# Performance work log

Hardware: AMD Instinct MI355X
Metric: run time of the kernel (lower is better)

The kernel has to match this reference:

```python
import jax, jax.numpy as jnp
import numpy as np

N_USERS = 200000
N_ITEMS = 200000
HOPS = 4      # n_hops + 1
DIM = 64
BATCH = 2048
N_NEGS = 64
K = 2
DECAY = 1e-4


def setup_inputs() -> dict:
    key = jax.random.key(0)
    k1, k2, k3, k4, k5, k6 = jax.random.split(key, 6)
    return {
        "user_gcn_emb": jax.random.normal(k1, (N_USERS, HOPS, DIM), dtype=jnp.float32),
        "item_gcn_emb": jax.random.normal(k2, (N_ITEMS, HOPS, DIM), dtype=jnp.float32),
        "seed_embed": jax.random.normal(k3, (BATCH, 1), dtype=jnp.float32),
        "user": jax.random.randint(k4, (BATCH,), 0, N_USERS, dtype=jnp.int64 if jax.config.jax_enable_x64 else jnp.int32),
        "pos_item": jax.random.randint(k5, (BATCH,), 0, N_ITEMS, dtype=jnp.int64 if jax.config.jax_enable_x64 else jnp.int32),
        "neg_item": jax.random.randint(k6, (BATCH, K * N_NEGS), 0, N_ITEMS, dtype=jnp.int64 if jax.config.jax_enable_x64 else jnp.int32),
    }


def _negative_sampling(user_gcn_emb, item_gcn_emb, user, neg_candidates, pos_item, seed_embed):
    # s_e, p_e: [B, H, C]; n_e: [B, N, H, C]
    s_e = user_gcn_emb[user]
    p_e = item_gcn_emb[pos_item]
    n_e = item_gcn_emb[neg_candidates]
    seed = seed_embed[:, :, None, None]                      # [B,1,1,1]
    # positive mixing
    n_e_ = seed * p_e[:, None, :, :] + (1.0 - seed) * n_e    # [B,N,H,C]
    # hop mixing: per-hop inner product scores
    scores = jnp.einsum("bhc,bnhc->bnh", s_e, n_e_)          # [B,N,H]
    idx = jnp.argmax(scores, axis=1)                         # [B,H] (detached/int)
    # select per-hop hardest mixed negative
    sel = jnp.take_along_axis(n_e_, idx[:, None, :, None], axis=1)  # [B,1,H,C]
    return sel[:, 0]                                         # [B,H,C]


def _bpr_loss(user_e, pos_e_hops, neg_e_hops):
    # user_e/pos_e_hops: [B,H,C]; neg_e_hops: [B,K,H,C]
    B = user_e.shape[0]
    u_e = jnp.mean(user_e, axis=1)          # [B,C]  (pool='mean')
    pos_e = jnp.mean(pos_e_hops, axis=1)    # [B,C]
    neg_e = jnp.mean(neg_e_hops, axis=2)    # [B,K,C]
    pos_scores = jnp.sum(u_e * pos_e, axis=-1)              # [B]
    neg_scores = jnp.einsum("bc,bkc->bk", u_e, neg_e)       # [B,K]
    mf_loss = jnp.mean(jnp.log1p(jnp.sum(jnp.exp(neg_scores - pos_scores[:, None]), axis=1)))
    regularize = (jnp.sum(u_e ** 2) + jnp.sum(pos_e ** 2) + jnp.sum(neg_e ** 2)) / 2.0
    emb_loss = DECAY * regularize / B
    return mf_loss + emb_loss, mf_loss, emb_loss


def reference(user_gcn_emb, item_gcn_emb, seed_embed, user, pos_item, neg_item):
    negs = []
    for k in range(K):
        negs.append(_negative_sampling(
            user_gcn_emb, item_gcn_emb, user,
            neg_item[:, k * N_NEGS:(k + 1) * N_NEGS], pos_item, seed_embed))
    neg_gcn_embs = jnp.stack(negs, axis=1)  # [B,K,H,C]
    loss, mf_loss, emb_loss = _bpr_loss(user_gcn_emb[user], item_gcn_emb[pos_item], neg_gcn_embs)
    return loss, mf_loss, emb_loss
```

## Files before the change

kernel.cpp:

```cpp
#include <hip/hip_runtime.h>
#include <math.h>

#define N_USERS 200000
#define N_ITEMS 200000
#define HOPS 4
#define DIM 64
#define BATCH 2048
#define N_NEGS 64
#define KK 2
#define ROW 256
#define DECAY 0.0001f

__global__ __launch_bounds__(256, 8) void mixgcf_main(
    const float* __restrict__ user_emb,
    const float* __restrict__ item_emb,
    const float* __restrict__ seed_embed,
    const int*   __restrict__ user,
    const int*   __restrict__ pos_item,
    const int*   __restrict__ neg_item,
    float*       __restrict__ ws)
{
    const int b    = blockIdx.x;
    const int tid  = threadIdx.x;
    const int w    = tid >> 6;
    const int lane = tid & 63;

    __shared__ int   nidx[KK * N_NEGS];
    __shared__ float selv[KK][ROW];
    __shared__ float scw[KK][4][HOPS];

    const int   uidx = user[b];
    const int   pidx = pos_item[b];
    const float seed = seed_embed[b];

    if (tid < KK * N_NEGS) nidx[tid] = neg_item[(size_t)b * (KK * N_NEGS) + tid];
    __syncthreads();

    const float4 s4 = *(const float4*)(user_emb + (size_t)uidx * ROW + lane * 4);
    const float4 p4 = *(const float4*)(item_emb + (size_t)pidx * ROW + lane * 4);
    const float  omse = 1.0f - seed;
    const float4 sp = make_float4(seed * p4.x, seed * p4.y, seed * p4.z, seed * p4.w);
    const int h = lane >> 4;

    float  best0 = -INFINITY, best1 = -INFINITY;
    float4 bv0 = make_float4(0.f, 0.f, 0.f, 0.f);
    float4 bv1 = make_float4(0.f, 0.f, 0.f, 0.f);

    #pragma unroll 8
    for (int i = 0; i < 16; ++i) {
        const int n   = (i << 2) + w;
        const int it0 = nidx[n];
        const int it1 = nidx[N_NEGS + n];
        const float4 ne0 = *(const float4*)(item_emb + (size_t)it0 * ROW + lane * 4);
        const float4 ne1 = *(const float4*)(item_emb + (size_t)it1 * ROW + lane * 4);

        float4 m0, m1;
        m0.x = fmaf(omse, ne0.x, sp.x); m1.x = fmaf(omse, ne1.x, sp.x);
        m0.y = fmaf(omse, ne0.y, sp.y); m1.y = fmaf(omse, ne1.y, sp.y);
        m0.z = fmaf(omse, ne0.z, sp.z); m1.z = fmaf(omse, ne1.z, sp.z);
        m0.w = fmaf(omse, ne0.w, sp.w); m1.w = fmaf(omse, ne1.w, sp.w);

        float sc0 = m0.x * s4.x;  float sc1 = m1.x * s4.x;
        sc0 = fmaf(m0.y, s4.y, sc0); sc1 = fmaf(m1.y, s4.y, sc1);
        sc0 = fmaf(m0.z, s4.z, sc0); sc1 = fmaf(m1.z, s4.z, sc1);
        sc0 = fmaf(m0.w, s4.w, sc0); sc1 = fmaf(m1.w, s4.w, sc1);

        sc0 += __shfl_xor(sc0, 1);  sc1 += __shfl_xor(sc1, 1);
        sc0 += __shfl_xor(sc0, 2);  sc1 += __shfl_xor(sc1, 2);
        sc0 += __shfl_xor(sc0, 4);  sc1 += __shfl_xor(sc1, 4);
        sc0 += __shfl_xor(sc0, 8);  sc1 += __shfl_xor(sc1, 8);

        if (sc0 > best0) { best0 = sc0; bv0 = m0; }
        if (sc1 > best1) { best1 = sc1; bv1 = m1; }
    }

    if ((lane & 15) == 0) { scw[0][w][h] = best0; scw[1][w][h] = best1; }
    __syncthreads();
    {
        float a0 = scw[0][0][h], a1 = scw[0][1][h], a2 = scw[0][2][h], a3 = scw[0][3][h];
        int win0 = 0; float mb = a0;
        if (a1 > mb) { mb = a1; win0 = 1; }
        if (a2 > mb) { mb = a2; win0 = 2; }
        if (a3 > mb) { mb = a3; win0 = 3; }
        if (w == win0) *(float4*)(&selv[0][lane * 4]) = bv0;

        float c0 = scw[1][0][h], c1 = scw[1][1][h], c2 = scw[1][2][h], c3 = scw[1][3][h];
        int win1 = 0; float nb = c0;
        if (c1 > nb) { nb = c1; win1 = 1; }
        if (c2 > nb) { nb = c2; win1 = 2; }
        if (c3 > nb) { nb = c3; win1 = 3; }
        if (w == win1) *(float4*)(&selv[1][lane * 4]) = bv1;
    }
    __syncthreads();

    if (w == 0) {
        const int c = lane;
        const float* ur = user_emb + (size_t)uidx * ROW;
        const float* pr = item_emb + (size_t)pidx * ROW;
        const float ue = 0.25f * (ur[c] + ur[64 + c] + ur[128 + c] + ur[192 + c]);
        const float pe = 0.25f * (pr[c] + pr[64 + c] + pr[128 + c] + pr[192 + c]);
        const float n0 = 0.25f * (selv[0][c] + selv[0][64 + c] + selv[0][128 + c] + selv[0][192 + c]);
        const float n1 = 0.25f * (selv[1][c] + selv[1][64 + c] + selv[1][128 + c] + selv[1][192 + c]);
        float ps  = ue * pe;
        float ns0 = ue * n0;
        float ns1 = ue * n1;
        float rg  = ue * ue + pe * pe + n0 * n0 + n1 * n1;
        #pragma unroll
        for (int m = 1; m < 64; m <<= 1) {
            ps  += __shfl_xor(ps,  m);
            ns0 += __shfl_xor(ns0, m);
            ns1 += __shfl_xor(ns1, m);
            rg  += __shfl_xor(rg,  m);
        }
        if (lane == 0) {
            const float mf = log1pf(expf(ns0 - ps) + expf(ns1 - ps));
            ws[b]         = mf;
            ws[BATCH + b] = rg;
        }
    }
}

__global__ __launch_bounds__(256) void mixgcf_reduce(const float* __restrict__ ws,
                                                     float* __restrict__ out)
{
    __shared__ float smf[256];
    __shared__ float srg[256];
    const int t = threadIdx.x;
    float mf = 0.f, rg = 0.f;
    #pragma unroll
    for (int i = 0; i < BATCH / 256; ++i) {
        mf += ws[t + i * 256];
        rg += ws[BATCH + t + i * 256];
    }
    smf[t] = mf; srg[t] = rg;
    __syncthreads();
    for (int s = 128; s > 0; s >>= 1) {
        if (t < s) { smf[t] += smf[t + s]; srg[t] += srg[t + s]; }
        __syncthreads();
    }
    if (t == 0) {
        const float mf_loss  = smf[0] / (float)BATCH;
        const float emb_loss = DECAY * (srg[0] * 0.5f) / (float)BATCH;
        out[0] = mf_loss + emb_loss;
        out[1] = mf_loss;
        out[2] = emb_loss;
    }
}

extern "C" void kernel_launch(void* const* d_in, const int* in_sizes, int n_in,
                              void* d_out, int out_size, void* d_ws, size_t ws_size,
                              hipStream_t stream)
{
    const float* user_emb  = (const float*)d_in[0];
    const float* item_emb  = (const float*)d_in[1];
    const float* seed      = (const float*)d_in[2];
    const int*   user      = (const int*)d_in[3];
    const int*   pos_item  = (const int*)d_in[4];
    const int*   neg_item  = (const int*)d_in[5];
    float* ws  = (float*)d_ws;
    float* out = (float*)d_out;

    mixgcf_main<<<BATCH, 256, 0, stream>>>(user_emb, item_emb, seed,
                                           user, pos_item, neg_item, ws);
    mixgcf_reduce<<<1, 256, 0, stream>>>(ws, out);
}
```

Before: 50.43 us.

## Stream negative item rows through an LDS ring via async global_load_lds

Replaces direct register gathers of negative item rows with asynchronous global-to-LDS loads into a 4-slot per-wave ring buffer, issuing three loads ahead and waiting with explicit vmcnt/lgkmcnt counters. The aim is to keep more gather requests in flight while cutting register pressure, so the memory-bound gather overlaps with compute. The cost is 16KB of LDS per block, which may lower occupancy below the 8-block launch bound. It also adds manual waitcnt handling, and the clamped tail issues redundant reloads of the last row into slots that might still be read.

```diff
diff --git a/kernel.cpp b/kernel.cpp
--- a/kernel.cpp
+++ b/kernel.cpp
@@ -25,6 +25,7 @@
     const int w    = tid >> 6;
     const int lane = tid & 63;
 
+    __shared__ float ring[4][4][ROW];
     __shared__ int   nidx[KK * N_NEGS];
     __shared__ float selv[KK][ROW];
     __shared__ float scw[KK][4][HOPS];
@@ -41,37 +42,56 @@
     const float  omse = 1.0f - seed;
     const float4 sp = make_float4(seed * p4.x, seed * p4.y, seed * p4.z, seed * p4.w);
     const int h = lane >> 4;
+    __builtin_amdgcn_sched_barrier(0);
+
+    auto issue = [&](int cc, int slot) {
+        const int k  = cc & 1;
+        const int i  = cc >> 1;
+        const int it = nidx[k * N_NEGS + (i << 2) + w];
+        const float* src = item_emb + (size_t)it * ROW + lane * 4;
+        __builtin_amdgcn_global_load_lds(
+            (const __attribute__((address_space(1))) void*)src,
+            (__attribute__((address_space(3))) void*)&ring[w][slot][0],
+            16, 0, 0);
+    };
+
+    issue(0, 0); issue(1, 1); issue(2, 2); issue(3, 3);
 
     float  best0 = -INFINITY, best1 = -INFINITY;
     float4 bv0 = make_float4(0.f, 0.f, 0.f, 0.f);
     float4 bv1 = make_float4(0.f, 0.f, 0.f, 0.f);
 
-    #pragma unroll 8
-    for (int i = 0; i < 16; ++i) {
-        const int n   = (i << 2) + w;
-        const int it0 = nidx[n];
-        const int it1 = nidx[N_NEGS + n];
-        const float4 ne0 = *(const float4*)(item_emb + (size_t)it0 * ROW + lane * 4);
-        const float4 ne1 = *(const float4*)(item_emb + (size_t)it1 * ROW + lane * 4);
+    #pragma unroll 4
+    for (int c = 0; c < 32; ++c) {
+        if (c > 0) {
+            asm volatile("s_waitcnt lgkmcnt(0)" ::: "memory");
+            __builtin_amdgcn_sched_barrier(0);
+            const int cc = (c + 3 < 32) ? (c + 3) : 31;
+            issue(cc, (c - 1) & 3);
+        }
+        asm volatile("s_waitcnt vmcnt(3)" ::: "memory");
+        __builtin_amdgcn_sched_barrier(0);
 
-        float4 m0, m1;
-        m0.x = fmaf(omse, ne0.x, sp.x); m1.x = fmaf(omse, ne1.x, sp.x);
-        m0.y = fmaf(omse, ne0.y, sp.y); m1.y = fmaf(omse, ne1.y, sp.y);
-        m0.z = fmaf(omse, ne0.z, sp.z); m1.z = fmaf(omse, ne1.z, sp.z);
-        m0.w = fmaf(omse, ne0.w, sp.w); m1.w = fmaf(omse, ne1.w, sp.w);
+        const int slot = c & 3;
+        const float4 ne = *(const float4*)&ring[w][slot][lane * 4];
 
-        float sc0 = m0.x * s4.x;  float sc1 = m1.x * s4.x;
-        sc0 = fmaf(m0.y, s4.y, sc0); sc1 = fmaf(m1.y, s4.y, sc1);
-        sc0 = fmaf(m0.z, s4.z, sc0); sc1 = fmaf(m1.z, s4.z, sc1);
-        sc0 = fmaf(m0.w, s4.w, sc0); sc1 = fmaf(m1.w, s4.w, sc1);
+        float4 m;
+        m.x = fmaf(omse, ne.x, sp.x);
+        m.y = fmaf(omse, ne.y, sp.y);
+        m.z = fmaf(omse, ne.z, sp.z);
+        m.w = fmaf(omse, ne.w, sp.w);
 
-        sc0 += __shfl_xor(sc0, 1);  sc1 += __shfl_xor(sc1, 1);
-        sc0 += __shfl_xor(sc0, 2);  sc1 += __shfl_xor(sc1, 2);
-        sc0 += __shfl_xor(sc0, 4);  sc1 += __shfl_xor(sc1, 4);
-        sc0 += __shfl_xor(sc0, 8);  sc1 += __shfl_xor(sc1, 8);
+        float sc = m.x * s4.x;
+        sc = fmaf(m.y, s4.y, sc);
+        sc = fmaf(m.z, s4.z, sc);
+        sc = fmaf(m.w, s4.w, sc);
+        sc += __shfl_xor(sc, 1);
+        sc += __shfl_xor(sc, 2);
+        sc += __shfl_xor(sc, 4);
+        sc += __shfl_xor(sc, 8);
 
-        if (sc0 > best0) { best0 = sc0; bv0 = m0; }
-        if (sc1 > best1) { best1 = sc1; bv1 = m1; }
+        if ((c & 1) == 0) { if (sc > best0) { best0 = sc; bv0 = m; } }
+        else              { if (sc > best1) { best1 = sc; bv1 = m; } }
     }
 
     if ((lane & 15) == 0) { scw[0][w][h] = best0; scw[1][w][h] = best1; }
```

After: 51.35 us. Within noise of the previous version (+1.8%).
